# Optimization experiments

Measured on AMD Instinct MI355X. Metric: run time of the kernel, lower is better.

Reference implementation:

```python
import jax, jax.numpy as jnp
import numpy as np

REACH = 2
BS = 32  # blocksize
NHID = 15  # nlayers - 1
CI = 12    # 2*(reach+1)*reach


def _offsets():
    # matches get_nb ordering: rows above (dy=-2,-1; dx=-2..2), then left (dy=0; dx=-2,-1)
    offs = [(dy, dx) for dy in range(-REACH, 0) for dx in range(-REACH, REACH + 1)]
    offs += [(0, dx) for dx in range(-REACH, 0)]
    return offs


def setup_inputs() -> dict:
    key = jax.random.key(0)
    k0, k1, k2, k3, k4 = jax.random.split(key, 5)
    x = jax.random.uniform(k0, (8, 3, 512, 512), jnp.float32, -1.0, 1.0)
    s = 1.0 / np.sqrt(CI).astype(np.float32)
    Wh = jax.random.uniform(k1, (NHID, CI, CI), jnp.float32, -s, s)
    bh = jax.random.uniform(k2, (NHID, CI), jnp.float32, -s, s)
    Wo = jax.random.uniform(k3, (1, CI), jnp.float32, -s, s)
    bo = jax.random.uniform(k4, (1,), jnp.float32, -s, s)
    return {"x": x, "Wh": Wh, "bh": bh, "Wo": Wo, "bo": bo}


def reference(x, Wh, bh, Wo, bo):
    b, c, h, w = x.shape
    h = h // BS * BS
    w = w // BS * BS
    x = x[:, :, :h, :w]
    nbh, nbw = h // BS, w // BS
    # unfold into (nbc, BS, BS) blocks, matching torch unfold/unfold/reshape
    blocks = x.reshape(b, c, nbh, BS, nbw, BS).transpose(0, 1, 2, 4, 3, 5).reshape(-1, BS, BS)
    xp = jnp.pad(blocks, ((0, 0), (REACH, REACH), (REACH, REACH)))
    # batched causal-neighbor gather: (nbc, BS, BS, 12)
    feats = jnp.stack(
        [xp[:, REACH + dy:REACH + dy + BS, REACH + dx:REACH + dx + BS] for dy, dx in _offsets()],
        axis=-1,
    )
    hdn = feats
    for l in range(NHID):
        hdn = jax.nn.leaky_relu(jnp.einsum('nhwi,oi->nhwo', hdn, Wh[l]) + bh[l])
    pred = jnp.clip(jnp.einsum('nhwi,oi->nhwo', hdn, Wo)[..., 0] + bo[0], -1.0, 1.0)
    deltas = jnp.fmod(blocks - pred + 1.0, 2.0) - 1.0
    deltas = deltas.reshape(b * c, h * w)
    loss1 = 255.0 * jnp.sqrt(jnp.mean(jnp.square(deltas)))
    return (loss1, deltas)
```

## Files before the change

### kernel.cpp

```cpp
#include <hip/hip_runtime.h>
#include <math.h>

#define CI 12
#define NHID 15
#define NBLK 6144
#define NPIX (NBLK * 1024)

typedef int i32x2 __attribute__((ext_vector_type(2)));

static __device__ __forceinline__ int h2pack(float lo, float hi) {
    auto h = __builtin_amdgcn_cvt_pkrtz(lo, hi);
    int r;
    __builtin_memcpy(&r, &h, 4);
    return r;
}

#define LKA \
  "v_cvt_pkrtz_f16_f32 v36, v44, v45\n" \
  "v_cvt_pkrtz_f16_f32 v37, v46, v47\n" \
  "v_pk_mul_f16 v60, s21, v36\n" \
  "v_pk_mul_f16 v61, s21, v37\n" \
  "v_pk_max_f16 v36, v36, v60\n" \
  "v_pk_max_f16 v37, v37, v61\n"
#define LKB \
  "v_cvt_pkrtz_f16_f32 v38, v48, v49\n" \
  "v_cvt_pkrtz_f16_f32 v39, v50, v51\n" \
  "v_pk_mul_f16 v60, s21, v38\n" \
  "v_pk_mul_f16 v61, s21, v39\n" \
  "v_pk_max_f16 v38, v38, v60\n" \
  "v_pk_max_f16 v39, v39, v61\n"
#define LKC \
  "v_cvt_pkrtz_f16_f32 v40, v52, v53\n" \
  "v_cvt_pkrtz_f16_f32 v41, v54, v55\n" \
  "v_pk_mul_f16 v60, s21, v40\n" \
  "v_pk_mul_f16 v61, s21, v41\n" \
  "v_pk_max_f16 v40, v40, v60\n" \
  "v_pk_max_f16 v41, v41, v61\n"
#define LKD \
  "v_cvt_pkrtz_f16_f32 v42, v56, v57\n" \
  "v_cvt_pkrtz_f16_f32 v43, v58, v59\n" \
  "v_pk_mul_f16 v60, s21, v42\n" \
  "v_pk_mul_f16 v61, s21, v43\n" \
  "v_pk_max_f16 v42, v42, v60\n" \
  "v_pk_max_f16 v43, v43, v61\n"

#define MFA(w) "v_mfma_f32_16x16x16_f16 v[44:47], %[" w "], v[36:37], v[32:35]\n"
#define MFB(w) "v_mfma_f32_16x16x16_f16 v[48:51], %[" w "], v[38:39], v[32:35]\n"
#define MFC(w) "v_mfma_f32_16x16x16_f16 v[52:55], %[" w "], v[40:41], v[32:35]\n"
#define MFD(w) "v_mfma_f32_16x16x16_f16 v[56:59], %[" w "], v[42:43], v[32:35]\n"

#define LAYER(w) LKA LKB MFA(w) LKC MFB(w) LKD MFC(w) "s_nop 1\n" MFD(w)

__global__ __launch_bounds__(256, 4) void codec_main(
    const float* __restrict__ x,
    const float* __restrict__ Wh,
    const float* __restrict__ bh,
    const float* __restrict__ Wo,
    const float* __restrict__ bo,
    float* __restrict__ out,
    float* __restrict__ loss_acc)
{
    __shared__ float tile[36 * 37];
    __shared__ float stage[4][256];
    __shared__ float wsum[4];

    const int n    = blockIdx.x;
    const int tid  = threadIdx.x;
    const int lane = tid & 63;
    const int wv   = tid >> 6;
    const int t    = lane & 15;
    const int q    = lane >> 4;

    {
        const int col = tid & 31;
        const int r0  = tid >> 5;
        #pragma unroll
        for (int i = 0; i < 6; ++i) {
            int idx = tid + i * 256;
            if (idx < 36 * 37) tile[idx] = 0.0f;
        }
        __syncthreads();
        const int bc  = n >> 8;
        const int blk = n & 255;
        const int by  = blk >> 4;
        const int bx  = blk & 15;
        #pragma unroll
        for (int p = 0; p < 4; ++p) {
            const int row = r0 + 8 * p;
            tile[(row + 2) * 37 + col + 2] =
                x[((size_t)bc * 512 + (size_t)(by * 32 + row)) * 512
                  + (size_t)(bx * 32 + col)];
        }
        __syncthreads();
    }

    i32x2 wq[16];
    #pragma unroll
    for (int l = 0; l < NHID; ++l) {
        int w0 = 0, w1 = 0;
        if (q < 3 && t < CI) {
            float4 w = *(const float4*)(Wh + l * (CI * CI) + t * CI + 4 * q);
            w0 = h2pack(w.x, w.y);
            w1 = h2pack(w.z, w.w);
        }
        if (q == 3 && t < CI)  w0 = h2pack(bh[l * CI + t], 0.f);
        if (q == 3 && t == CI) w0 = 0x3C00;
        wq[l] = (i32x2){ w0, w1 };
    }
    {
        int w0 = 0, w1 = 0;
        if (t == 0 && q < 3) {
            float4 w = *(const float4*)(Wo + 4 * q);
            w0 = h2pack(w.x, w.y);
            w1 = h2pack(w.z, w.w);
        }
        if (t == 0 && q == 3) w0 = h2pack(bo[0], 0.f);
        wq[15] = (i32x2){ w0, w1 };
    }

    const int sh8  = q * 8;
    const int off0 = (int)(signed char)((0x00DCB8B4u >> sh8) & 0xFFu);
    const int off1 = (int)(signed char)((0x00DDD9B5u >> sh8) & 0xFFu);
    const int off2 = (int)(signed char)((0x00FEDAB6u >> sh8) & 0xFFu);
    const int off3 = (int)(signed char)((0x00FFDBB7u >> sh8) & 0xFFu);
    const bool q3  = (q == 3);

    int e = (wv * 8 + 2) * 37 + (t + 2);

    float d2 = 0.0f;
    #pragma unroll 1
    for (int yi = 0; yi < 4; ++yi) {
        const int faA0 = q3 ? 0x3C00 : h2pack(tile[e + off0],      tile[e + off1]);
        const int faA1 = q3 ? 0      : h2pack(tile[e + off2],      tile[e + off3]);
        const int fbA0 = q3 ? 0x3C00 : h2pack(tile[e + off0 + 16], tile[e + off1 + 16]);
        const int fbA1 = q3 ? 0      : h2pack(tile[e + off2 + 16], tile[e + off3 + 16]);
        const int fcA0 = q3 ? 0x3C00 : h2pack(tile[e + off0 + 37], tile[e + off1 + 37]);
        const int fcA1 = q3 ? 0      : h2pack(tile[e + off2 + 37], tile[e + off3 + 37]);
        const int fdA0 = q3 ? 0x3C00 : h2pack(tile[e + off0 + 53], tile[e + off1 + 53]);
        const int fdA1 = q3 ? 0      : h2pack(tile[e + off2 + 53], tile[e + off3 + 53]);
        const float vA = tile[e], vB = tile[e + 16];
        const float vC = tile[e + 37], vD = tile[e + 53];

        float pA, pB, pC, pD;
        asm volatile(
            "s_mov_b32 s21, 0x211f211f\n"
            "v_mov_b32 v32, 0\n" "v_mov_b32 v33, 0\n"
            "v_mov_b32 v34, 0\n" "v_mov_b32 v35, 0\n"
            "v_mov_b32 v36, %[fa0]\n" "v_mov_b32 v37, %[fa1]\n"
            "v_mov_b32 v38, %[fb0]\n" "v_mov_b32 v39, %[fb1]\n"
            "v_mov_b32 v40, %[fc0]\n" "v_mov_b32 v41, %[fc1]\n"
            "v_mov_b32 v42, %[fd0]\n" "v_mov_b32 v43, %[fd1]\n"
            MFA("w0") MFB("w0") MFC("w0") MFD("w0")
            "s_nop 7\n" "s_nop 7\n" "s_nop 7\n" "s_nop 4\n"
            LAYER("w1")  LAYER("w2")  LAYER("w3")  LAYER("w4")
            LAYER("w5")  LAYER("w6")  LAYER("w7")  LAYER("w8")
            LAYER("w9")  LAYER("w10") LAYER("w11") LAYER("w12")
            LAYER("w13") LAYER("w14") LAYER("w15")
            "v_mov_b32 %[pA], v44\n"
            "s_nop 1\n"
            "v_mov_b32 %[pB], v48\n"
            "s_nop 7\n" "s_nop 7\n"
            "v_mov_b32 %[pC], v52\n"
            "s_nop 3\n"
            "v_mov_b32 %[pD], v56\n"
            : [pA] "=v"(pA), [pB] "=v"(pB), [pC] "=v"(pC), [pD] "=v"(pD)
            : [w0] "a"(wq[0]),  [w1] "a"(wq[1]),  [w2] "a"(wq[2]),
              [w3] "a"(wq[3]),  [w4] "a"(wq[4]),  [w5] "a"(wq[5]),
              [w6] "a"(wq[6]),  [w7] "a"(wq[7]),  [w8] "a"(wq[8]),
              [w9] "a"(wq[9]),  [w10] "a"(wq[10]), [w11] "a"(wq[11]),
              [w12] "a"(wq[12]), [w13] "a"(wq[13]), [w14] "a"(wq[14]),
              [w15] "a"(wq[15]),
              [fa0] "v"(faA0), [fa1] "v"(faA1), [fb0] "v"(fbA0), [fb1] "v"(fbA1),
              [fc0] "v"(fcA0), [fc1] "v"(fcA1), [fd0] "v"(fdA0), [fd1] "v"(fdA1)
            : "s21",
              "v32","v33","v34","v35","v36","v37","v38","v39",
              "v40","v41","v42","v43","v44","v45","v46","v47",
              "v48","v49","v50","v51","v52","v53","v54","v55",
              "v56","v57","v58","v59","v60","v61");

        if (lane < 16) {
            const float qA = fminf(fmaxf(pA, -1.0f), 1.0f);
            const float uA = vA - qA + 1.0f;
            const float dA = uA - ((uA < 2.0f) ? 1.0f : 3.0f);
            const float qB = fminf(fmaxf(pB, -1.0f), 1.0f);
            const float uB = vB - qB + 1.0f;
            const float dB = uB - ((uB < 2.0f) ? 1.0f : 3.0f);
            const float qC = fminf(fmaxf(pC, -1.0f), 1.0f);
            const float uC = vC - qC + 1.0f;
            const float dC = uC - ((uC < 2.0f) ? 1.0f : 3.0f);
            const float qD = fminf(fmaxf(pD, -1.0f), 1.0f);
            const float uD = vD - qD + 1.0f;
            const float dD = uD - ((uD < 2.0f) ? 1.0f : 3.0f);
            const int r = 2 * yi;
            stage[wv][r * 32 + t]            = dA;
            stage[wv][r * 32 + 16 + t]       = dB;
            stage[wv][(r + 1) * 32 + t]      = dC;
            stage[wv][(r + 1) * 32 + 16 + t] = dD;
            d2 = fmaf(dA, dA, fmaf(dB, dB, fmaf(dC, dC, fmaf(dD, dD, d2))));
        }
        e += 74;
    }

    float* outp = out + 1 + (size_t)n * 1024 + wv * 256;
    #pragma unroll
    for (int j = 0; j < 4; ++j)
        outp[j * 64 + lane] = stage[wv][j * 64 + lane];

    #pragma unroll
    for (int off = 8; off > 0; off >>= 1) d2 += __shfl_down(d2, off, 64);
    if (lane == 0) wsum[wv] = d2;
    __syncthreads();
    if (tid == 0) atomicAdd(loss_acc, wsum[0] + wsum[1] + wsum[2] + wsum[3]);
}

__global__ void codec_loss(const float* __restrict__ acc, float* __restrict__ out)
{
    out[0] = 255.0f * sqrtf(acc[0] / (float)NPIX);
}

extern "C" void kernel_launch(void* const* d_in, const int* in_sizes, int n_in,
                              void* d_out, int out_size, void* d_ws, size_t ws_size,
                              hipStream_t stream)
{
    const float* x  = (const float*)d_in[0];
    const float* Wh = (const float*)d_in[1];
    const float* bh = (const float*)d_in[2];
    const float* Wo = (const float*)d_in[3];
    const float* bo = (const float*)d_in[4];
    float* out = (float*)d_out;
    float* acc = (float*)d_ws;

    hipMemsetAsync(acc, 0, sizeof(float), stream);
    codec_main<<<NBLK, 256, 0, stream>>>(x, Wh, bh, Wo, bo, out, acc);
    codec_loss<<<1, 1, 0, stream>>>(acc, out);
}
```

Before: 183.7 us.

## Prefetch next row's LDS features with ds_read2 during MFMA chain

Reorders the feature (K) dimension so the neighbour gathers pair up into adjacent or fixed-stride LDS addresses, which can then be fetched with ds_read2_b32 using immediate offsets. The weight packing is permuted to match the new K order. Features for the next row pair are issued before the inline-asm MLP chain and waited on afterwards, so LDS latency is hidden behind the MFMA layers. This costs more live VGPRs, and the last iteration issues a redundant reload of the current row.

```diff
diff --git a/kernel.cpp b/kernel.cpp
--- a/kernel.cpp
+++ b/kernel.cpp
@@ -6,7 +6,8 @@
 #define NBLK 6144
 #define NPIX (NBLK * 1024)
 
-typedef int i32x2 __attribute__((ext_vector_type(2)));
+typedef int   i32x2 __attribute__((ext_vector_type(2)));
+typedef float f32x2 __attribute__((ext_vector_type(2)));
 
 static __device__ __forceinline__ int h2pack(float lo, float hi) {
     auto h = __builtin_amdgcn_cvt_pkrtz(lo, hi);
@@ -51,6 +52,37 @@
 
 #define LAYER(w) LKA LKB MFA(w) LKC MFB(w) LKD MFC(w) "s_nop 1\n" MFD(w)
 
+#define DSLOADS(EN) do {                                                      \
+    const unsigned aA = ldsbase + (unsigned)(((EN) + offA) * 4);              \
+    const unsigned aB = ldsbase + (unsigned)(((EN) + offB) * 4);              \
+    const unsigned aV = ldsbase + (unsigned)((EN) * 4);                       \
+    asm volatile("ds_read2_b32 %0, %1 offset0:0 offset1:1"   : "=v"(a01) : "v"(aA)); \
+    asm volatile("ds_read2_b32 %0, %1 offset0:16 offset1:17" : "=v"(a23) : "v"(aA)); \
+    asm volatile("ds_read2_b32 %0, %1 offset0:37 offset1:38" : "=v"(a45) : "v"(aA)); \
+    asm volatile("ds_read2_b32 %0, %1 offset0:53 offset1:54" : "=v"(a67) : "v"(aA)); \
+    asm volatile("ds_read2_b32 %0, %1 offset0:0 offset1:37"  : "=v"(b02) : "v"(aB)); \
+    asm volatile("ds_read2_b32 %0, %1 offset0:16 offset1:53" : "=v"(b13) : "v"(aB)); \
+    asm volatile("ds_read2_b32 %0, %1 offset0:74 offset1:90" : "=v"(b45) : "v"(aB)); \
+    asm volatile("ds_read2_b32 %0, %1 offset0:0 offset1:16"  : "=v"(v01) : "v"(aV)); \
+    asm volatile("ds_read2_b32 %0, %1 offset0:37 offset1:53" : "=v"(v23) : "v"(aV)); \
+} while (0)
+
+#define DSWAIT() asm volatile("s_waitcnt lgkmcnt(0)"                          \
+    : "+v"(a01), "+v"(a23), "+v"(a45), "+v"(a67),                             \
+      "+v"(b02), "+v"(b13), "+v"(b45), "+v"(v01), "+v"(v23))
+
+#define PACKF() do {                                                          \
+    fa0 = q3 ? 0x3C00 : h2pack(a01.x, a01.y);                                 \
+    fb0 = q3 ? 0x3C00 : h2pack(a23.x, a23.y);                                 \
+    fc0 = q3 ? 0x3C00 : h2pack(a45.x, a45.y);                                 \
+    fd0 = q3 ? 0x3C00 : h2pack(a67.x, a67.y);                                 \
+    fa1 = q3 ? 0 : h2pack(b02.x, b02.y);                                      \
+    fb1 = q3 ? 0 : h2pack(b13.x, b13.y);                                      \
+    fc1 = q3 ? 0 : h2pack(b02.y, b45.x);                                      \
+    fd1 = q3 ? 0 : h2pack(b13.y, b45.y);                                      \
+    vA = v01.x; vB = v01.y; vC = v23.x; vD = v23.y;                           \
+} while (0)
+
 __global__ __launch_bounds__(256, 4) void codec_main(
     const float* __restrict__ x,
     const float* __restrict__ Wh,
@@ -94,14 +126,15 @@
         __syncthreads();
     }
 
+    const int kA = (q == 0) ? 3 : (q == 1) ? 8 : 10;
     i32x2 wq[16];
     #pragma unroll
     for (int l = 0; l < NHID; ++l) {
         int w0 = 0, w1 = 0;
         if (q < 3 && t < CI) {
-            float4 w = *(const float4*)(Wh + l * (CI * CI) + t * CI + 4 * q);
-            w0 = h2pack(w.x, w.y);
-            w1 = h2pack(w.z, w.w);
+            const float* wr = Wh + l * (CI * CI) + t * CI;
+            w0 = h2pack(wr[kA], wr[kA + 1]);
+            w1 = h2pack(wr[q],  wr[q + 5]);
         }
         if (q == 3 && t < CI)  w0 = h2pack(bh[l * CI + t], 0.f);
         if (q == 3 && t == CI) w0 = 0x3C00;
@@ -110,36 +143,34 @@
     {
         int w0 = 0, w1 = 0;
         if (t == 0 && q < 3) {
-            float4 w = *(const float4*)(Wo + 4 * q);
-            w0 = h2pack(w.x, w.y);
-            w1 = h2pack(w.z, w.w);
+            w0 = h2pack(Wo[kA], Wo[kA + 1]);
+            w1 = h2pack(Wo[q],  Wo[q + 5]);
         }
         if (t == 0 && q == 3) w0 = h2pack(bo[0], 0.f);
         wq[15] = (i32x2){ w0, w1 };
     }
 
     const int sh8  = q * 8;
-    const int off0 = (int)(signed char)((0x00DCB8B4u >> sh8) & 0xFFu);
-    const int off1 = (int)(signed char)((0x00DDD9B5u >> sh8) & 0xFFu);
-    const int off2 = (int)(signed char)((0x00FEDAB6u >> sh8) & 0xFFu);
-    const int off3 = (int)(signed char)((0x00FFDBB7u >> sh8) & 0xFFu);
+    const int offA = (int)(signed char)((0x00FEDCB7u >> sh8) & 0xFFu);
+    const int offB = (int)(signed char)((0x00B6B5B4u >> sh8) & 0xFFu);
     const bool q3  = (q == 3);
+    const unsigned ldsbase = (unsigned)(uintptr_t)(&tile[0]);
 
     int e = (wv * 8 + 2) * 37 + (t + 2);
+
+    f32x2 a01, a23, a45, a67, b02, b13, b45, v01, v23;
+    int fa0, fa1, fb0, fb1, fc0, fc1, fd0, fd1;
+    float vA, vB, vC, vD;
+
+    DSLOADS(e);
+    DSWAIT();
+    PACKF();
 
     float d2 = 0.0f;
     #pragma unroll 1
     for (int yi = 0; yi < 4; ++yi) {
-        const int faA0 = q3 ? 0x3C00 : h2pack(tile[e + off0],      tile[e + off1]);
-        const int faA1 = q3 ? 0      : h2pack(tile[e + off2],      tile[e + off3]);
-        const int fbA0 = q3 ? 0x3C00 : h2pack(tile[e + off0 + 16], tile[e + off1 + 16]);
-        const int fbA1 = q3 ? 0      : h2pack(tile[e + off2 + 16], tile[e + off3 + 16]);
-        const int fcA0 = q3 ? 0x3C00 : h2pack(tile[e + off0 + 37], tile[e + off1 + 37]);
-        const int fcA1 = q3 ? 0      : h2pack(tile[e + off2 + 37], tile[e + off3 + 37]);
-        const int fdA0 = q3 ? 0x3C00 : h2pack(tile[e + off0 + 53], tile[e + off1 + 53]);
-        const int fdA1 = q3 ? 0      : h2pack(tile[e + off2 + 53], tile[e + off3 + 53]);
-        const float vA = tile[e], vB = tile[e + 16];
-        const float vC = tile[e + 37], vD = tile[e + 53];
+        const int en = (yi < 3) ? e + 74 : e;
+        DSLOADS(en);
 
         float pA, pB, pC, pD;
         asm volatile(
@@ -170,13 +201,15 @@
               [w9] "a"(wq[9]),  [w10] "a"(wq[10]), [w11] "a"(wq[11]),
               [w12] "a"(wq[12]), [w13] "a"(wq[13]), [w14] "a"(wq[14]),
               [w15] "a"(wq[15]),
-              [fa0] "v"(faA0), [fa1] "v"(faA1), [fb0] "v"(fbA0), [fb1] "v"(fbA1),
-              [fc0] "v"(fcA0), [fc1] "v"(fcA1), [fd0] "v"(fdA0), [fd1] "v"(fdA1)
+              [fa0] "v"(fa0), [fa1] "v"(fa1), [fb0] "v"(fb0), [fb1] "v"(fb1),
+              [fc0] "v"(fc0), [fc1] "v"(fc1), [fd0] "v"(fd0), [fd1] "v"(fd1)
             : "s21",
               "v32","v33","v34","v35","v36","v37","v38","v39",
               "v40","v41","v42","v43","v44","v45","v46","v47",
               "v48","v49","v50","v51","v52","v53","v54","v55",
               "v56","v57","v58","v59","v60","v61");
+
+        DSWAIT();
 
         if (lane < 16) {
             const float qA = fminf(fmaxf(pA, -1.0f), 1.0f);
@@ -198,7 +231,8 @@
             stage[wv][(r + 1) * 32 + 16 + t] = dD;
             d2 = fmaf(dA, dA, fmaf(dB, dB, fmaf(dC, dC, fmaf(dD, dD, d2))));
         }
-        e += 74;
+        e = en;
+        PACKF();
     }
 
     float* outp = out + 1 + (size_t)n * 1024 + wv * 256;
```

Result: slower. 192.2 us (+4.7%).

## Make main kernel persistent with double-buffered tile prefetch across blocks

Applied to the files above, without the earlier changes.

The grid shrinks to 1024 workgroups, and each one processes six image blocks in sequence. The next block's pixels are loaded into registers while the current block's MLP runs, then written into the other shared-memory tile buffer. This amortizes the weight packing and tile zeroing per workgroup and hides the global load latency. It also means a single atomic per workgroup. The cost is more LDS per workgroup and fewer workgroups in flight, which may reduce occupancy-based latency hiding. There is also a hazard: the stage buffer is reused across iterations, and the only barrier comes after the next tile is written.

```diff
diff --git a/kernel.cpp b/kernel.cpp
--- a/kernel.cpp
+++ b/kernel.cpp
@@ -4,7 +4,10 @@
 #define CI 12
 #define NHID 15
 #define NBLK 6144
+#define GRID 1024
+#define ITERS 6
 #define NPIX (NBLK * 1024)
+#define TSZ (36 * 37)
 
 typedef int i32x2 __attribute__((ext_vector_type(2)));
 
@@ -60,38 +63,23 @@
     float* __restrict__ out,
     float* __restrict__ loss_acc)
 {
-    __shared__ float tile[36 * 37];
+    __shared__ float tile[2][TSZ];
     __shared__ float stage[4][256];
     __shared__ float wsum[4];
 
-    const int n    = blockIdx.x;
+    const int bid  = blockIdx.x;
     const int tid  = threadIdx.x;
     const int lane = tid & 63;
     const int wv   = tid >> 6;
     const int t    = lane & 15;
     const int q    = lane >> 4;
-
-    {
-        const int col = tid & 31;
-        const int r0  = tid >> 5;
-        #pragma unroll
-        for (int i = 0; i < 6; ++i) {
-            int idx = tid + i * 256;
-            if (idx < 36 * 37) tile[idx] = 0.0f;
-        }
-        __syncthreads();
-        const int bc  = n >> 8;
-        const int blk = n & 255;
-        const int by  = blk >> 4;
-        const int bx  = blk & 15;
-        #pragma unroll
-        for (int p = 0; p < 4; ++p) {
-            const int row = r0 + 8 * p;
-            tile[(row + 2) * 37 + col + 2] =
-                x[((size_t)bc * 512 + (size_t)(by * 32 + row)) * 512
-                  + (size_t)(bx * 32 + col)];
-        }
-        __syncthreads();
+    const int col  = tid & 31;
+    const int r0   = tid >> 5;
+
+    #pragma unroll
+    for (int i = 0; i < 11; ++i) {
+        int idx = tid + i * 256;
+        if (idx < 2 * TSZ) ((float*)tile)[idx] = 0.0f;
     }
 
     i32x2 wq[16];
@@ -125,86 +113,129 @@
     const int off3 = (int)(signed char)((0x00FFDBB7u >> sh8) & 0xFFu);
     const bool q3  = (q == 3);
 
-    int e = (wv * 8 + 2) * 37 + (t + 2);
-
+    __syncthreads();
+
+    {
+        const int bc = bid >> 8, blk = bid & 255, by = blk >> 4, bx = blk & 15;
+        #pragma unroll
+        for (int p = 0; p < 4; ++p) {
+            const int row = r0 + 8 * p;
+            tile[0][(row + 2) * 37 + col + 2] =
+                x[((size_t)bc * 512 + (size_t)(by * 32 + row)) * 512
+                  + (size_t)(bx * 32 + col)];
+        }
+    }
+    __syncthreads();
+
+    const int ebase = (wv * 8 + 2) * 37 + (t + 2);
     float d2 = 0.0f;
+
     #pragma unroll 1
-    for (int yi = 0; yi < 4; ++yi) {
-        const int faA0 = q3 ? 0x3C00 : h2pack(tile[e + off0],      tile[e + off1]);
-        const int faA1 = q3 ? 0      : h2pack(tile[e + off2],      tile[e + off3]);
-        const int fbA0 = q3 ? 0x3C00 : h2pack(tile[e + off0 + 16], tile[e + off1 + 16]);
-        const int fbA1 = q3 ? 0      : h2pack(tile[e + off2 + 16], tile[e + off3 + 16]);
-        const int fcA0 = q3 ? 0x3C00 : h2pack(tile[e + off0 + 37], tile[e + off1 + 37]);
-        const int fcA1 = q3 ? 0      : h2pack(tile[e + off2 + 37], tile[e + off3 + 37]);
-        const int fdA0 = q3 ? 0x3C00 : h2pack(tile[e + off0 + 53], tile[e + off1 + 53]);
-        const int fdA1 = q3 ? 0      : h2pack(tile[e + off2 + 53], tile[e + off3 + 53]);
-        const float vA = tile[e], vB = tile[e + 16];
-        const float vC = tile[e + 37], vD = tile[e + 53];
-
-        float pA, pB, pC, pD;
-        asm volatile(
-            "s_mov_b32 s21, 0x211f211f\n"
-            "v_mov_b32 v32, 0\n" "v_mov_b32 v33, 0\n"
-            "v_mov_b32 v34, 0\n" "v_mov_b32 v35, 0\n"
-            "v_mov_b32 v36, %[fa0]\n" "v_mov_b32 v37, %[fa1]\n"
-            "v_mov_b32 v38, %[fb0]\n" "v_mov_b32 v39, %[fb1]\n"
-            "v_mov_b32 v40, %[fc0]\n" "v_mov_b32 v41, %[fc1]\n"
-            "v_mov_b32 v42, %[fd0]\n" "v_mov_b32 v43, %[fd1]\n"
-            MFA("w0") MFB("w0") MFC("w0") MFD("w0")
-            "s_nop 7\n" "s_nop 7\n" "s_nop 7\n" "s_nop 4\n"
-            LAYER("w1")  LAYER("w2")  LAYER("w3")  LAYER("w4")
-            LAYER("w5")  LAYER("w6")  LAYER("w7")  LAYER("w8")
-            LAYER("w9")  LAYER("w10") LAYER("w11") LAYER("w12")
-            LAYER("w13") LAYER("w14") LAYER("w15")
-            "v_mov_b32 %[pA], v44\n"
-            "s_nop 1\n"
-            "v_mov_b32 %[pB], v48\n"
-            "s_nop 7\n" "s_nop 7\n"
-            "v_mov_b32 %[pC], v52\n"
-            "s_nop 3\n"
-            "v_mov_b32 %[pD], v56\n"
-            : [pA] "=v"(pA), [pB] "=v"(pB), [pC] "=v"(pC), [pD] "=v"(pD)
-            : [w0] "a"(wq[0]),  [w1] "a"(wq[1]),  [w2] "a"(wq[2]),
-              [w3] "a"(wq[3]),  [w4] "a"(wq[4]),  [w5] "a"(wq[5]),
-              [w6] "a"(wq[6]),  [w7] "a"(wq[7]),  [w8] "a"(wq[8]),
-              [w9] "a"(wq[9]),  [w10] "a"(wq[10]), [w11] "a"(wq[11]),
-              [w12] "a"(wq[12]), [w13] "a"(wq[13]), [w14] "a"(wq[14]),
-              [w15] "a"(wq[15]),
-              [fa0] "v"(faA0), [fa1] "v"(faA1), [fb0] "v"(fbA0), [fb1] "v"(fbA1),
-              [fc0] "v"(fcA0), [fc1] "v"(fcA1), [fd0] "v"(fdA0), [fd1] "v"(fdA1)
-            : "s21",
-              "v32","v33","v34","v35","v36","v37","v38","v39",
-              "v40","v41","v42","v43","v44","v45","v46","v47",
-              "v48","v49","v50","v51","v52","v53","v54","v55",
-              "v56","v57","v58","v59","v60","v61");
-
-        if (lane < 16) {
-            const float qA = fminf(fmaxf(pA, -1.0f), 1.0f);
-            const float uA = vA - qA + 1.0f;
-            const float dA = uA - ((uA < 2.0f) ? 1.0f : 3.0f);
-            const float qB = fminf(fmaxf(pB, -1.0f), 1.0f);
-            const float uB = vB - qB + 1.0f;
-            const float dB = uB - ((uB < 2.0f) ? 1.0f : 3.0f);
-            const float qC = fminf(fmaxf(pC, -1.0f), 1.0f);
-            const float uC = vC - qC + 1.0f;
-            const float dC = uC - ((uC < 2.0f) ? 1.0f : 3.0f);
-            const float qD = fminf(fmaxf(pD, -1.0f), 1.0f);
-            const float uD = vD - qD + 1.0f;
-            const float dD = uD - ((uD < 2.0f) ? 1.0f : 3.0f);
-            const int r = 2 * yi;
-            stage[wv][r * 32 + t]            = dA;
-            stage[wv][r * 32 + 16 + t]       = dB;
-            stage[wv][(r + 1) * 32 + t]      = dC;
-            stage[wv][(r + 1) * 32 + 16 + t] = dD;
-            d2 = fmaf(dA, dA, fmaf(dB, dB, fmaf(dC, dC, fmaf(dD, dD, d2))));
-        }
-        e += 74;
-    }
-
-    float* outp = out + 1 + (size_t)n * 1024 + wv * 256;
-    #pragma unroll
-    for (int j = 0; j < 4; ++j)
-        outp[j * 64 + lane] = stage[wv][j * 64 + lane];
+    for (int it = 0; it < ITERS; ++it) {
+        const int cur = it & 1;
+        const float* tl = &tile[cur][0];
+        const int n = bid + it * GRID;
+
+        float nx0 = 0.f, nx1 = 0.f, nx2 = 0.f, nx3 = 0.f;
+        if (it + 1 < ITERS) {
+            const int nn = n + GRID;
+            const int bc = nn >> 8, blk = nn & 255, by = blk >> 4, bx = blk & 15;
+            const float* xp = x + ((size_t)bc * 512 + (size_t)(by * 32 + r0)) * 512
+                                + (size_t)(bx * 32 + col);
+            nx0 = xp[0];
+            nx1 = xp[8 * 512];
+            nx2 = xp[16 * 512];
+            nx3 = xp[24 * 512];
+        }
+
+        int e = ebase;
+        #pragma unroll 1
+        for (int yi = 0; yi < 4; ++yi) {
+            const int faA0 = q3 ? 0x3C00 : h2pack(tl[e + off0],      tl[e + off1]);
+            const int faA1 = q3 ? 0      : h2pack(tl[e + off2],      tl[e + off3]);
+            const int fbA0 = q3 ? 0x3C00 : h2pack(tl[e + off0 + 16], tl[e + off1 + 16]);
+            const int fbA1 = q3 ? 0      : h2pack(tl[e + off2 + 16], tl[e + off3 + 16]);
+            const int fcA0 = q3 ? 0x3C00 : h2pack(tl[e + off0 + 37], tl[e + off1 + 37]);
+            const int fcA1 = q3 ? 0      : h2pack(tl[e + off2 + 37], tl[e + off3 + 37]);
+            const int fdA0 = q3 ? 0x3C00 : h2pack(tl[e + off0 + 53], tl[e + off1 + 53]);
+            const int fdA1 = q3 ? 0      : h2pack(tl[e + off2 + 53], tl[e + off3 + 53]);
+            const float vA = tl[e], vB = tl[e + 16];
+            const float vC = tl[e + 37], vD = tl[e + 53];
+
+            float pA, pB, pC, pD;
+            asm volatile(
+                "s_mov_b32 s21, 0x211f211f\n"
+                "v_mov_b32 v32, 0\n" "v_mov_b32 v33, 0\n"
+                "v_mov_b32 v34, 0\n" "v_mov_b32 v35, 0\n"
+                "v_mov_b32 v36, %[fa0]\n" "v_mov_b32 v37, %[fa1]\n"
+                "v_mov_b32 v38, %[fb0]\n" "v_mov_b32 v39, %[fb1]\n"
+                "v_mov_b32 v40, %[fc0]\n" "v_mov_b32 v41, %[fc1]\n"
+                "v_mov_b32 v42, %[fd0]\n" "v_mov_b32 v43, %[fd1]\n"
+                MFA("w0") MFB("w0") MFC("w0") MFD("w0")
+                "s_nop 7\n" "s_nop 7\n" "s_nop 7\n" "s_nop 4\n"
+                LAYER("w1")  LAYER("w2")  LAYER("w3")  LAYER("w4")
+                LAYER("w5")  LAYER("w6")  LAYER("w7")  LAYER("w8")
+                LAYER("w9")  LAYER("w10") LAYER("w11") LAYER("w12")
+                LAYER("w13") LAYER("w14") LAYER("w15")
+                "v_mov_b32 %[pA], v44\n"
+                "s_nop 1\n"
+                "v_mov_b32 %[pB], v48\n"
+                "s_nop 7\n" "s_nop 7\n"
+                "v_mov_b32 %[pC], v52\n"
+                "s_nop 3\n"
+                "v_mov_b32 %[pD], v56\n"
+                : [pA] "=v"(pA), [pB] "=v"(pB), [pC] "=v"(pC), [pD] "=v"(pD)
+                : [w0] "a"(wq[0]),  [w1] "a"(wq[1]),  [w2] "a"(wq[2]),
+                  [w3] "a"(wq[3]),  [w4] "a"(wq[4]),  [w5] "a"(wq[5]),
+                  [w6] "a"(wq[6]),  [w7] "a"(wq[7]),  [w8] "a"(wq[8]),
+                  [w9] "a"(wq[9]),  [w10] "a"(wq[10]), [w11] "a"(wq[11]),
+                  [w12] "a"(wq[12]), [w13] "a"(wq[13]), [w14] "a"(wq[14]),
+                  [w15] "a"(wq[15]),
+                  [fa0] "v"(faA0), [fa1] "v"(faA1), [fb0] "v"(fbA0), [fb1] "v"(fbA1),
+                  [fc0] "v"(fcA0), [fc1] "v"(fcA1), [fd0] "v"(fdA0), [fd1] "v"(fdA1)
+                : "s21",
+                  "v32","v33","v34","v35","v36","v37","v38","v39",
+                  "v40","v41","v42","v43","v44","v45","v46","v47",
+                  "v48","v49","v50","v51","v52","v53","v54","v55",
+                  "v56","v57","v58","v59","v60","v61");
+
+            if (lane < 16) {
+                const float qA = fminf(fmaxf(pA, -1.0f), 1.0f);
+                const float uA = vA - qA + 1.0f;
+                const float dA = uA - ((uA < 2.0f) ? 1.0f : 3.0f);
+                const float qB = fminf(fmaxf(pB, -1.0f), 1.0f);
+                const float uB = vB - qB + 1.0f;
+                const float dB = uB - ((uB < 2.0f) ? 1.0f : 3.0f);
+                const float qC = fminf(fmaxf(pC, -1.0f), 1.0f);
+                const float uC = vC - qC + 1.0f;
+                const float dC = uC - ((uC < 2.0f) ? 1.0f : 3.0f);
+                const float qD = fminf(fmaxf(pD, -1.0f), 1.0f);
+                const float uD = vD - qD + 1.0f;
+                const float dD = uD - ((uD < 2.0f) ? 1.0f : 3.0f);
+                const int r = 2 * yi;
+                stage[wv][r * 32 + t]            = dA;
+                stage[wv][r * 32 + 16 + t]       = dB;
+                stage[wv][(r + 1) * 32 + t]      = dC;
+                stage[wv][(r + 1) * 32 + 16 + t] = dD;
+                d2 = fmaf(dA, dA, fmaf(dB, dB, fmaf(dC, dC, fmaf(dD, dD, d2))));
+            }
+            e += 74;
+        }
+
+        float* outp = out + 1 + (size_t)n * 1024 + wv * 256;
+        #pragma unroll
+        for (int j = 0; j < 4; ++j)
+            outp[j * 64 + lane] = stage[wv][j * 64 + lane];
+
+        if (it + 1 < ITERS) {
+            float* nt = &tile[cur ^ 1][0];
+            nt[(r0 + 2)  * 37 + col + 2] = nx0;
+            nt[(r0 + 10) * 37 + col + 2] = nx1;
+            nt[(r0 + 18) * 37 + col + 2] = nx2;
+            nt[(r0 + 26) * 37 + col + 2] = nx3;
+            __syncthreads();
+        }
+    }
 
     #pragma unroll
     for (int off = 8; off > 0; off >>= 1) d2 += __shfl_down(d2, off, 64);
@@ -231,6 +262,6 @@
     float* acc = (float*)d_ws;
 
     hipMemsetAsync(acc, 0, sizeof(float), stream);
-    codec_main<<<NBLK, 256, 0, stream>>>(x, Wh, bh, Wo, bo, out, acc);
+    codec_main<<<GRID, 256, 0, stream>>>(x, Wh, bh, Wo, bo, out, acc);
     codec_loss<<<1, 1, 0, stream>>>(acc, out);
 }
```

Result: no change. 183.9 us (+0.1%).
